# Optimization experiments

Hardware: AMD Instinct MI355X
Metric: run time of the kernel (lower is better)

Reference implementation:

```python
import jax, jax.numpy as jnp
import numpy as np

D_MODEL = 128
D_STATE = 16
BATCH = 4
SEQ = 4096
LOG_CLAMP = 70.0  # numeric floor used by the original (use_double=False path)


def setup_inputs() -> dict:
    key = jax.random.key(0)
    ks = jax.random.split(key, 10)
    sd = 1.0 / np.sqrt(D_MODEL)
    x = jax.random.normal(ks[0], (BATCH, SEQ, D_MODEL), dtype=jnp.float32)
    # Araw: kaiming-normal then clamped at min=-4
    Araw = jnp.clip(jax.random.normal(ks[1], (D_MODEL, D_STATE), dtype=jnp.float32) * np.sqrt(2.0 / D_MODEL), -4.0, None)
    P = jax.random.normal(ks[2], (D_MODEL,), dtype=jnp.float32)
    W_B = jax.random.normal(ks[3], (D_MODEL, D_STATE), dtype=jnp.float32) * sd
    b_B = jax.random.normal(ks[4], (D_STATE,), dtype=jnp.float32) * sd
    W_C = jax.random.normal(ks[5], (D_MODEL, D_STATE), dtype=jnp.float32) * sd
    b_C = jax.random.normal(ks[6], (D_STATE,), dtype=jnp.float32) * sd
    W_D = jax.random.normal(ks[7], (D_MODEL, 1), dtype=jnp.float32) * sd
    b_D = jax.random.normal(ks[8], (1,), dtype=jnp.float32) * sd
    return {"x": x, "Araw": Araw, "P": P, "W_B": W_B, "b_B": b_B,
            "W_C": W_C, "b_C": b_C, "W_D": W_D, "b_D": b_D}


def reference(x, Araw, P, W_B, b_B, W_C, b_C, W_D, b_D):
    sp = jax.nn.softplus
    # disc: [B,S,D] -- s_D(x) is [B,S,1], repeated across d_model == broadcast
    disc = sp(P + (x @ W_D + b_D))
    A = -sp(Araw)                          # [D,N], strictly negative
    A_bar_pre = disc[..., None] * A        # [B,S,D,N] (log of A_bar)
    A_bar = jnp.exp(A_bar_pre)             # [B,S,D,N]
    Bm = x @ W_B + b_B                     # [B,S,N]
    B_bar = Bm[:, :, None, :] / A * (A_bar - 1.0)  # [B,S,D,N]
    C = x @ W_C + b_C                      # [B,S,N]

    # log-space parallel scan (pref_sum path, use_double=False)
    Bx = B_bar * x[..., None]              # [B,S,D,N]
    Bx_log = jnp.log(jnp.abs(Bx))
    A_bar_prod_log = jnp.cumsum(A_bar_pre, axis=1)          # inclusive prefix sum of logs
    A_bar_prod_log = jnp.maximum(A_bar_prod_log, Bx_log - LOG_CLAMP)
    AinvsB = jnp.exp(Bx_log - A_bar_prod_log) * jnp.sign(Bx)
    AinvsBsum = jnp.cumsum(AinvsB, axis=1)
    h = AinvsBsum * jnp.exp(A_bar_prod_log)                 # [B,S,D,N]
    y = jnp.einsum('bsdn,bsn->bsd', h, C)                   # [B,S,D]
    return y
```

## Files before the change

### kernel.cpp

```cpp
#include <hip/hip_runtime.h>
#include <math.h>

#define B_ 4
#define S_ 4096
#define D_ 128
#define N_ 16
#define CHUNK_ 64
#define NCHUNK_ (S_ / CHUNK_)
#define NCHAN_ (B_ * D_ * N_)
#define KC_ 8
#define KNC_ (S_ / KC_)

#define CAPF  3.0e38f
#define LOG2E 1.4426950408889634f
#define C70F  100.98865286222744f

__device__ __forceinline__ float fast_sp(float z) {
    return fmaxf(z, 0.0f) + __logf(1.0f + __expf(-fabsf(z)));
}

__device__ __forceinline__ float exp2_hw(float x) {
#if __has_builtin(__builtin_amdgcn_exp2f)
    return __builtin_amdgcn_exp2f(x);
#else
    return exp2f(x);
#endif
}

template<int CTRL>
__device__ __forceinline__ float dpp_radd(float v) {
    int o = __builtin_amdgcn_mov_dpp(__float_as_int(v), CTRL, 0xf, 0xf, true);
    return v + __int_as_float(o);
}

__device__ __forceinline__ float dpp_reduce16(float v) {
    v = dpp_radd<0x121>(v);
    v = dpp_radd<0x122>(v);
    v = dpp_radd<0x124>(v);
    v = dpp_radd<0x128>(v);
    return v;
}

__global__ __launch_bounds__(256) void k1_proj(
    const float* __restrict__ x,
    const float* __restrict__ W_B, const float* __restrict__ b_B,
    const float* __restrict__ W_C, const float* __restrict__ b_C,
    const float* __restrict__ W_D, const float* __restrict__ b_D,
    float* __restrict__ xWD, float* __restrict__ BmT, float* __restrict__ CmT)
{
    __shared__ float xs[16][132];
    __shared__ float sB[16][17], sC[16][17];
    const int row0 = blockIdx.x * 16;
    const int b  = row0 >> 12;
    const int t0 = row0 & (S_ - 1);
    const int tid = threadIdx.x;

    {
        const float4* xsrc = (const float4*)(x + (size_t)row0 * D_);
        int i0 = tid * 2;
        float4 v0 = xsrc[i0];
        float4 v1 = xsrc[i0 + 1];
        int r = i0 >> 5;
        int c = (i0 << 2) & 127;
        *(float4*)&xs[r][c]     = v0;
        *(float4*)&xs[r][c + 4] = v1;
    }
    __syncthreads();

    const int r = tid >> 4;
    const int n = tid & 15;
    float a = 0.f, c = 0.f;
    #pragma unroll 4
    for (int k = 0; k < D_; ++k) {
        float xv = xs[r][k];
        a = fmaf(xv, W_B[k * N_ + n], a);
        c = fmaf(xv, W_C[k * N_ + n], c);
    }
    sB[n][r] = a + b_B[n];
    sC[n][r] = c + b_C[n];

    if (tid < 16) {
        float dsum = 0.f;
        #pragma unroll 4
        for (int k = 0; k < D_; ++k) dsum = fmaf(xs[tid][k], W_D[k], dsum);
        xWD[row0 + tid] = dsum + b_D[0];
    }
    __syncthreads();

    const int n2 = tid >> 4, r2 = tid & 15;
    BmT[(size_t)(b * N_ + n2) * S_ + t0 + r2] = sB[n2][r2];
    CmT[(size_t)(b * N_ + n2) * S_ + t0 + r2] = sC[n2][r2];
}

__global__ __launch_bounds__(512) void kS(
    const float* __restrict__ xWD, const float* __restrict__ P,
    float* __restrict__ dstart)
{
    __shared__ float wtot[8];
    const int bd = blockIdx.x;
    const int b = bd >> 7, d = bd & (D_ - 1);
    const float Pd = P[d];
    const int c = threadIdx.x;
    const int lane = c & 63, wv = c >> 6;

    const float4* xw = (const float4*)(xWD + b * S_) + c * 2;
    float4 a0 = xw[0], a1 = xw[1];
    float s = fast_sp(Pd + a0.x) + fast_sp(Pd + a0.y)
            + fast_sp(Pd + a0.z) + fast_sp(Pd + a0.w)
            + fast_sp(Pd + a1.x) + fast_sp(Pd + a1.y)
            + fast_sp(Pd + a1.z) + fast_sp(Pd + a1.w);
    float sc = s;
    #pragma unroll
    for (int off = 1; off < 64; off <<= 1) {
        float o = __shfl_up(sc, off);
        if (lane >= off) sc += o;
    }
    if (lane == 63) wtot[wv] = sc;
    __syncthreads();
    float base = 0.f;
    #pragma unroll
    for (int i = 0; i < 7; ++i)
        if (i < wv) base += wtot[i];
    dstart[bd * KNC_ + c] = base + sc - s;
}

template <int PHASE_C>
__global__ __launch_bounds__(256, 8) void k3_scan(
    const float* __restrict__ x, const float* __restrict__ Araw,
    const float* __restrict__ P, const float* __restrict__ xWD,
    const float* __restrict__ BmT, const float* __restrict__ CmT,
    const float* __restrict__ dstart,
    float* __restrict__ csum,
    float* __restrict__ y)
{
    __shared__ __align__(16) float lds[PHASE_C ? 5 * 1024 : 3 * 1024 + 64];
    float* ld_x = lds;
    float* ld_b = lds + 1024;
    float* ld_d = lds + 2048;
    float* ld_c = lds + (PHASE_C ? 3072 : 0);
    float* ld_y = lds + (PHASE_C ? 4096 : 0);

    const int blk = blockIdx.x;
    const int dg = blk & 7;
    const int ch = (blk >> 3) & (NCHUNK_ - 1);
    const int b  = blk >> 9;
    const int tid = threadIdx.x;
    const int lane = tid & 63;
    const int w = tid >> 6;
    const int n  = tid & 15;
    const int dl = tid >> 4;
    const int d  = dg * 16 + dl;
    const int bd = b * D_ + d;
    const int cid = bd * N_ + n;
    const int t0 = ch * CHUNK_;

    float carry = 0.f;
    if (PHASE_C) {
        float p0 = 0.f, p1 = 0.f, p2 = 0.f, p3 = 0.f;
        int k = 0;
        for (; k + 4 <= ch; k += 4) {
            p0 += csum[(size_t)(k + 0) * NCHAN_ + cid];
            p1 += csum[(size_t)(k + 1) * NCHAN_ + cid];
            p2 += csum[(size_t)(k + 2) * NCHAN_ + cid];
            p3 += csum[(size_t)(k + 3) * NCHAN_ + cid];
        }
        for (; k < ch; ++k) p0 += csum[(size_t)k * NCHAN_ + cid];
        carry = (p0 + p1) + (p2 + p3);
    }

    if (w == 0) {
        const float* src = x + ((size_t)b * S_ + t0) * D_ + dg * 16;
        #pragma unroll
        for (int it = 0; it < 4; ++it) {
            int g = it * 64 + lane;
            int t = g >> 2, dq = g & 3;
            float4 v = *(const float4*)(src + (size_t)t * D_ + dq * 4);
            int t4 = t >> 2, tl = t & 3;
            const float va[4] = {v.x, v.y, v.z, v.w};
            #pragma unroll
            for (int j = 0; j < 4; ++j) {
                int dd = dq * 4 + j;
                ld_x[dd * 64 + ((t4 ^ (dd & 7)) << 2) + tl] = va[j];
            }
        }
    } else if (w == 1) {
        const float* src = BmT + (size_t)(b * N_) * S_ + t0;
        #pragma unroll
        for (int it = 0; it < 4; ++it) {
            int g = it * 64 + lane;
            int row = g >> 4, t16 = g & 15;
            int tlog = t16 ^ (row & 7);
            *(float4*)&ld_b[row * 64 + t16 * 4] =
                *(const float4*)(src + (size_t)row * S_ + tlog * 4);
        }
    } else if (PHASE_C && w == 2) {
        const float* src = CmT + (size_t)(b * N_) * S_ + t0;
        #pragma unroll
        for (int it = 0; it < 4; ++it) {
            int g = it * 64 + lane;
            int row = g >> 4, t16 = g & 15;
            int tlog = t16 ^ (row & 7);
            *(float4*)&ld_c[row * 64 + t16 * 4] =
                *(const float4*)(src + (size_t)row * S_ + tlog * 4);
        }
    } else if (w == (PHASE_C ? 3 : 2)) {
        float v = xWD[b * S_ + t0 + lane];
        int t4 = lane >> 2, tl = lane & 3;
        #pragma unroll
        for (int dl2 = 0; dl2 < 16; ++dl2) {
            float sp = fast_sp(P[dg * 16 + dl2] + v);
            ld_d[dl2 * 64 + ((t4 ^ (dl2 & 7)) << 2) + tl] = sp;
        }
    }
    __syncthreads();

    if (!PHASE_C) {
        unsigned long long* mk = (unsigned long long*)(lds + 3072);
        #pragma unroll
        for (int i = 0; i < 4; ++i) {
            int rr = w * 4 + i;
            int idx = rr * 64 + ((((lane >> 2) ^ (rr & 7)) << 2) | (lane & 3));
            unsigned long long mx = __ballot((__float_as_uint(ld_x[idx]) >> 31) & 1);
            unsigned long long mb = __ballot((__float_as_uint(ld_b[idx]) >> 31) & 1);
            if (lane == 0) { mk[rr] = mx; mk[16 + rr] = mb; }
        }
        __syncthreads();
    }

    const float A  = -fast_sp(Araw[d * N_ + n]);
    const float rA = 1.0f / A;
    const float A2 = A * LOG2E;

    const float cum0 = fmaf(A2, dstart[bd * KNC_ + ch * (CHUNK_ / KC_)], C70F);
    float cum2 = cum0;
    float run = carry;

    const int sdl = dl & 7, sn = n & 7;
    const int offd_base = dl * 64;
    const int offn_base = n * 64;

    const bool fastp = __all(cum0 <= -128.0f);

    if (fastp) {
        if (!PHASE_C) {
            const unsigned long long* mk =
                (const unsigned long long*)(lds + 3072);
            int pc = (int)__popcll(mk[dl] ^ mk[16 + n]);
            run += (float)(64 - 2 * pc);
        } else {
            #pragma unroll 2
            for (int t4 = 0; t4 < CHUNK_ / 4; ++t4) {
                const int od = offd_base + ((t4 ^ sdl) << 2);
                const int on = offn_base + ((t4 ^ sn) << 2);
                float4 dv = *(const float4*)&ld_d[od];
                float4 xv = *(const float4*)&ld_x[od];
                float4 bv = *(const float4*)&ld_b[on];
                float4 Cv = *(const float4*)&ld_c[on];
                const float dva[4] = {dv.x, dv.y, dv.z, dv.w};
                const float xva[4] = {xv.x, xv.y, xv.z, xv.w};
                const float bva[4] = {bv.x, bv.y, bv.z, bv.w};
                const float Cva[4] = {Cv.x, Cv.y, Cv.z, Cv.w};
                #pragma unroll
                for (int j = 0; j < 4; ++j) {
                    float ab  = exp2_hw(dva[j] * A2);
                    float ww  = fmaf(ab, xva[j], -xva[j]);
                    float Bx  = (bva[j] * rA) * ww;
                    run += copysignf(1.0f, Bx);
                    float yv = run * fabsf(Bx) * Cva[j];
                    yv = dpp_reduce16(yv);
                    if (n == 0) ld_y[(t4 * 4 + j) * 16 + dl] = yv;
                }
            }
        }
    } else {
        #pragma unroll 2
        for (int t4 = 0; t4 < CHUNK_ / 4; ++t4) {
            const int od = offd_base + ((t4 ^ sdl) << 2);
            const int on = offn_base + ((t4 ^ sn) << 2);
            float4 dv = *(const float4*)&ld_d[od];
            float4 xv = *(const float4*)&ld_x[od];
            float4 bv = *(const float4*)&ld_b[on];
            float4 Cv;
            if (PHASE_C) Cv = *(const float4*)&ld_c[on];

            const float dva[4] = {dv.x, dv.y, dv.z, dv.w};
            const float xva[4] = {xv.x, xv.y, xv.z, xv.w};
            const float bva[4] = {bv.x, bv.y, bv.z, bv.w};
            const float Cva[4] = {Cv.x, Cv.y, Cv.z, Cv.w};

            #pragma unroll
            for (int j = 0; j < 4; ++j) {
                float t1 = dva[j] * A2;
                cum2 += t1;
                float ab  = exp2_hw(t1);
                float ww  = fmaf(ab, xva[j], -xva[j]);
                float Bx  = (bva[j] * rA) * ww;
                float aBx = fabsf(Bx);
                float en  = fminf(exp2_hw(-cum2), CAPF);
                float m   = aBx * en;
                float mag = fminf(m, 1.0f);
                run += copysignf(mag, Bx);
                if (PHASE_C) {
                    float ecl = aBx * __builtin_amdgcn_rcpf(fmaxf(mag, 1e-37f));
                    float yv = run * ecl * Cva[j];
                    yv = dpp_reduce16(yv);
                    if (n == 0) ld_y[(t4 * 4 + j) * 16 + dl] = yv;
                }
            }
        }
    }

    if (!PHASE_C) {
        csum[(size_t)ch * NCHAN_ + cid] = run;
    } else {
        __syncthreads();
        int t  = tid >> 2;
        int dp = tid & 3;
        float4 v = *(const float4*)&ld_y[t * 16 + dp * 4];
        *(float4*)&y[((size_t)b * S_ + t0 + t) * D_ + dg * 16 + dp * 4] = v;
    }
}

extern "C" void kernel_launch(void* const* d_in, const int* in_sizes, int n_in,
                              void* d_out, int out_size, void* d_ws, size_t ws_size,
                              hipStream_t stream)
{
    const float* x    = (const float*)d_in[0];
    const float* Araw = (const float*)d_in[1];
    const float* P    = (const float*)d_in[2];
    const float* W_B  = (const float*)d_in[3];
    const float* b_B  = (const float*)d_in[4];
    const float* W_C  = (const float*)d_in[5];
    const float* b_C  = (const float*)d_in[6];
    const float* W_D  = (const float*)d_in[7];
    const float* b_D  = (const float*)d_in[8];
    float* y  = (float*)d_out;
    float* ws = (float*)d_ws;

    float* xWD    = ws;
    float* BmT    = xWD  + B_ * S_;
    float* CmT    = BmT  + B_ * S_ * N_;
    float* dstart = CmT  + B_ * S_ * N_;
    float* csum   = dstart + B_ * D_ * KNC_;

    hipLaunchKernelGGL(k1_proj, dim3(B_ * S_ / 16), dim3(256), 0, stream,
                       x, W_B, b_B, W_C, b_C, W_D, b_D, xWD, BmT, CmT);
    hipLaunchKernelGGL(kS, dim3(B_ * D_), dim3(512), 0, stream,
                       xWD, P, dstart);
    hipLaunchKernelGGL((k3_scan<0>), dim3(B_ * NCHUNK_ * (D_ / 16)), dim3(256), 0, stream,
                       x, Araw, P, xWD, BmT, CmT, dstart, csum, y);
    hipLaunchKernelGGL((k3_scan<1>), dim3(B_ * NCHUNK_ * (D_ / 16)), dim3(256), 0, stream,
                       x, Araw, P, xWD, BmT, CmT, dstart, csum, y);
}
```

Before: 60.39 us.

## Fuse two scan phases into one cooperative kernel with grid sync

Merges the chunk-sum phase and the output phase of the scan into a single cooperative kernel separated by a grid-wide barrier. Inputs stay staged in LDS across both phases instead of being reloaded by a second launch. The aim is to save one kernel launch plus the repeated global-to-LDS staging. In exchange it pays for a grid sync across 2048 blocks and host-side occupancy queries on every call, and it falls back to the old two-kernel path if a cooperative launch is not possible.

After: 60.57 us. Within noise of the previous version (+0.3%).

```diff
diff --git a/kernel.cpp b/kernel.cpp
--- a/kernel.cpp
+++ b/kernel.cpp
@@ -1,5 +1,8 @@
 #include <hip/hip_runtime.h>
+#include <hip/hip_cooperative_groups.h>
 #include <math.h>
+
+namespace cg = cooperative_groups;
 
 #define B_ 4
 #define S_ 4096
@@ -7,6 +10,7 @@
 #define N_ 16
 #define CHUNK_ 64
 #define NCHUNK_ (S_ / CHUNK_)
+#define NTASK_ (B_ * 8 * NCHUNK_)
 #define NCHAN_ (B_ * D_ * N_)
 #define KC_ 8
 #define KNC_ (S_ / KC_)
@@ -124,8 +128,53 @@
     dstart[bd * KNC_ + c] = base + sc - s;
 }
 
-template <int PHASE_C>
-__global__ __launch_bounds__(256, 8) void k3_scan(
+__device__ __forceinline__ void stage_x(
+    const float* __restrict__ x, float* ld_x,
+    int b, int t0, int dg, int lane)
+{
+    const float* src = x + ((size_t)b * S_ + t0) * D_ + dg * 16;
+    #pragma unroll
+    for (int it = 0; it < 4; ++it) {
+        int g = it * 64 + lane;
+        int t = g >> 2, dq = g & 3;
+        float4 v = *(const float4*)(src + (size_t)t * D_ + dq * 4);
+        int t4 = t >> 2, tl = t & 3;
+        const float va[4] = {v.x, v.y, v.z, v.w};
+        #pragma unroll
+        for (int j = 0; j < 4; ++j) {
+            int dd = dq * 4 + j;
+            ld_x[dd * 64 + ((t4 ^ (dd & 7)) << 2) + tl] = va[j];
+        }
+    }
+}
+
+__device__ __forceinline__ void stage_rowmajor(
+    const float* __restrict__ src, float* dst, int lane)
+{
+    #pragma unroll
+    for (int it = 0; it < 4; ++it) {
+        int g = it * 64 + lane;
+        int row = g >> 4, t16 = g & 15;
+        int tlog = t16 ^ (row & 7);
+        *(float4*)&dst[row * 64 + t16 * 4] =
+            *(const float4*)(src + (size_t)row * S_ + tlog * 4);
+    }
+}
+
+__device__ __forceinline__ void stage_disc(
+    const float* __restrict__ xWD, const float* __restrict__ P,
+    float* ld_d, int b, int t0, int dg, int lane)
+{
+    float v = xWD[b * S_ + t0 + lane];
+    int t4 = lane >> 2, tl = lane & 3;
+    #pragma unroll
+    for (int dl2 = 0; dl2 < 16; ++dl2) {
+        float sp = fast_sp(P[dg * 16 + dl2] + v);
+        ld_d[dl2 * 64 + ((t4 ^ (dl2 & 7)) << 2) + tl] = sp;
+    }
+}
+
+__global__ __launch_bounds__(256, 8) void k3_fused(
     const float* __restrict__ x, const float* __restrict__ Araw,
     const float* __restrict__ P, const float* __restrict__ xWD,
     const float* __restrict__ BmT, const float* __restrict__ CmT,
@@ -133,12 +182,12 @@
     float* __restrict__ csum,
     float* __restrict__ y)
 {
-    __shared__ __align__(16) float lds[PHASE_C ? 5 * 1024 : 3 * 1024 + 64];
+    __shared__ __align__(16) float lds[5 * 1024];
     float* ld_x = lds;
     float* ld_b = lds + 1024;
     float* ld_d = lds + 2048;
-    float* ld_c = lds + (PHASE_C ? 3072 : 0);
-    float* ld_y = lds + (PHASE_C ? 4096 : 0);
+    float* ld_c = lds + 3072;
+    float* ld_y = lds + 4096;
 
     const int blk = blockIdx.x;
     const int dg = blk & 7;
@@ -154,6 +203,185 @@
     const int cid = bd * N_ + n;
     const int t0 = ch * CHUNK_;
 
+    if (w == 0)      stage_x(x, ld_x, b, t0, dg, lane);
+    else if (w == 1) stage_rowmajor(BmT + (size_t)(b * N_) * S_ + t0, ld_b, lane);
+    else if (w == 2) stage_rowmajor(CmT + (size_t)(b * N_) * S_ + t0, ld_c, lane);
+    else             stage_disc(xWD, P, ld_d, b, t0, dg, lane);
+    __syncthreads();
+
+    {
+        unsigned long long* mk = (unsigned long long*)ld_y;
+        #pragma unroll
+        for (int i = 0; i < 4; ++i) {
+            int rr = w * 4 + i;
+            int idx = rr * 64 + ((((lane >> 2) ^ (rr & 7)) << 2) | (lane & 3));
+            unsigned long long mx = __ballot((__float_as_uint(ld_x[idx]) >> 31) & 1);
+            unsigned long long mb = __ballot((__float_as_uint(ld_b[idx]) >> 31) & 1);
+            if (lane == 0) { mk[rr] = mx; mk[16 + rr] = mb; }
+        }
+        __syncthreads();
+    }
+
+    const float A  = -fast_sp(Araw[d * N_ + n]);
+    const float rA = 1.0f / A;
+    const float A2 = A * LOG2E;
+    const float cum0 = fmaf(A2, dstart[bd * KNC_ + ch * (CHUNK_ / KC_)], C70F);
+
+    const int sdl = dl & 7, sn = n & 7;
+    const int offd_base = dl * 64;
+    const int offn_base = n * 64;
+    const bool fastp = __all(cum0 <= -128.0f);
+
+    {
+        float run0 = 0.f;
+        if (fastp) {
+            const unsigned long long* mk = (const unsigned long long*)ld_y;
+            int pc = (int)__popcll(mk[dl] ^ mk[16 + n]);
+            run0 = (float)(64 - 2 * pc);
+        } else {
+            float cum2 = cum0;
+            #pragma unroll 2
+            for (int t4 = 0; t4 < CHUNK_ / 4; ++t4) {
+                const int od = offd_base + ((t4 ^ sdl) << 2);
+                const int on = offn_base + ((t4 ^ sn) << 2);
+                float4 dv = *(const float4*)&ld_d[od];
+                float4 xv = *(const float4*)&ld_x[od];
+                float4 bv = *(const float4*)&ld_b[on];
+                const float dva[4] = {dv.x, dv.y, dv.z, dv.w};
+                const float xva[4] = {xv.x, xv.y, xv.z, xv.w};
+                const float bva[4] = {bv.x, bv.y, bv.z, bv.w};
+                #pragma unroll
+                for (int j = 0; j < 4; ++j) {
+                    float t1 = dva[j] * A2;
+                    cum2 += t1;
+                    float ab  = exp2_hw(t1);
+                    float ww  = fmaf(ab, xva[j], -xva[j]);
+                    float Bx  = (bva[j] * rA) * ww;
+                    float en  = fminf(exp2_hw(-cum2), CAPF);
+                    float m   = fabsf(Bx) * en;
+                    run0 += copysignf(fminf(m, 1.0f), Bx);
+                }
+            }
+        }
+        csum[(size_t)ch * NCHAN_ + cid] = run0;
+    }
+
+    __threadfence();
+    cg::this_grid().sync();
+    __threadfence();
+
+    float carry = 0.f;
+    {
+        float p0 = 0.f, p1 = 0.f, p2 = 0.f, p3 = 0.f;
+        int k = 0;
+        for (; k + 4 <= ch; k += 4) {
+            p0 += csum[(size_t)(k + 0) * NCHAN_ + cid];
+            p1 += csum[(size_t)(k + 1) * NCHAN_ + cid];
+            p2 += csum[(size_t)(k + 2) * NCHAN_ + cid];
+            p3 += csum[(size_t)(k + 3) * NCHAN_ + cid];
+        }
+        for (; k < ch; ++k) p0 += csum[(size_t)k * NCHAN_ + cid];
+        carry = (p0 + p1) + (p2 + p3);
+    }
+
+    float run = carry;
+    float cum2 = cum0;
+    if (fastp) {
+        #pragma unroll 2
+        for (int t4 = 0; t4 < CHUNK_ / 4; ++t4) {
+            const int od = offd_base + ((t4 ^ sdl) << 2);
+            const int on = offn_base + ((t4 ^ sn) << 2);
+            float4 dv = *(const float4*)&ld_d[od];
+            float4 xv = *(const float4*)&ld_x[od];
+            float4 bv = *(const float4*)&ld_b[on];
+            float4 Cv = *(const float4*)&ld_c[on];
+            const float dva[4] = {dv.x, dv.y, dv.z, dv.w};
+            const float xva[4] = {xv.x, xv.y, xv.z, xv.w};
+            const float bva[4] = {bv.x, bv.y, bv.z, bv.w};
+            const float Cva[4] = {Cv.x, Cv.y, Cv.z, Cv.w};
+            #pragma unroll
+            for (int j = 0; j < 4; ++j) {
+                float ab  = exp2_hw(dva[j] * A2);
+                float ww  = fmaf(ab, xva[j], -xva[j]);
+                float Bx  = (bva[j] * rA) * ww;
+                run += copysignf(1.0f, Bx);
+                float yv = run * fabsf(Bx) * Cva[j];
+                yv = dpp_reduce16(yv);
+                if (n == 0) ld_y[(t4 * 4 + j) * 16 + dl] = yv;
+            }
+        }
+    } else {
+        #pragma unroll 2
+        for (int t4 = 0; t4 < CHUNK_ / 4; ++t4) {
+            const int od = offd_base + ((t4 ^ sdl) << 2);
+            const int on = offn_base + ((t4 ^ sn) << 2);
+            float4 dv = *(const float4*)&ld_d[od];
+            float4 xv = *(const float4*)&ld_x[od];
+            float4 bv = *(const float4*)&ld_b[on];
+            float4 Cv = *(const float4*)&ld_c[on];
+            const float dva[4] = {dv.x, dv.y, dv.z, dv.w};
+            const float xva[4] = {xv.x, xv.y, xv.z, xv.w};
+            const float bva[4] = {bv.x, bv.y, bv.z, bv.w};
+            const float Cva[4] = {Cv.x, Cv.y, Cv.z, Cv.w};
+            #pragma unroll
+            for (int j = 0; j < 4; ++j) {
+                float t1 = dva[j] * A2;
+                cum2 += t1;
+                float ab  = exp2_hw(t1);
+                float ww  = fmaf(ab, xva[j], -xva[j]);
+                float Bx  = (bva[j] * rA) * ww;
+                float aBx = fabsf(Bx);
+                float en  = fminf(exp2_hw(-cum2), CAPF);
+                float m   = aBx * en;
+                float mag = fminf(m, 1.0f);
+                run += copysignf(mag, Bx);
+                float ecl = aBx * __builtin_amdgcn_rcpf(fmaxf(mag, 1e-37f));
+                float yv = run * ecl * Cva[j];
+                yv = dpp_reduce16(yv);
+                if (n == 0) ld_y[(t4 * 4 + j) * 16 + dl] = yv;
+            }
+        }
+    }
+
+    __syncthreads();
+    {
+        int t  = tid >> 2;
+        int dp = tid & 3;
+        float4 v = *(const float4*)&ld_y[t * 16 + dp * 4];
+        *(float4*)&y[((size_t)b * S_ + t0 + t) * D_ + dg * 16 + dp * 4] = v;
+    }
+}
+
+template <int PHASE_C>
+__global__ __launch_bounds__(256, 8) void k3_scan(
+    const float* __restrict__ x, const float* __restrict__ Araw,
+    const float* __restrict__ P, const float* __restrict__ xWD,
+    const float* __restrict__ BmT, const float* __restrict__ CmT,
+    const float* __restrict__ dstart,
+    float* __restrict__ csum,
+    float* __restrict__ y)
+{
+    __shared__ __align__(16) float lds[PHASE_C ? 5 * 1024 : 3 * 1024 + 64];
+    float* ld_x = lds;
+    float* ld_b = lds + 1024;
+    float* ld_d = lds + 2048;
+    float* ld_c = lds + (PHASE_C ? 3072 : 0);
+    float* ld_y = lds + (PHASE_C ? 4096 : 0);
+
+    const int blk = blockIdx.x;
+    const int dg = blk & 7;
+    const int ch = (blk >> 3) & (NCHUNK_ - 1);
+    const int b  = blk >> 9;
+    const int tid = threadIdx.x;
+    const int lane = tid & 63;
+    const int w = tid >> 6;
+    const int n  = tid & 15;
+    const int dl = tid >> 4;
+    const int d  = dg * 16 + dl;
+    const int bd = b * D_ + d;
+    const int cid = bd * N_ + n;
+    const int t0 = ch * CHUNK_;
+
     float carry = 0.f;
     if (PHASE_C) {
         float p0 = 0.f, p1 = 0.f, p2 = 0.f, p3 = 0.f;
@@ -168,50 +396,12 @@
         carry = (p0 + p1) + (p2 + p3);
     }
 
-    if (w == 0) {
-        const float* src = x + ((size_t)b * S_ + t0) * D_ + dg * 16;
-        #pragma unroll
-        for (int it = 0; it < 4; ++it) {
-            int g = it * 64 + lane;
-            int t = g >> 2, dq = g & 3;
-            float4 v = *(const float4*)(src + (size_t)t * D_ + dq * 4);
-            int t4 = t >> 2, tl = t & 3;
-            const float va[4] = {v.x, v.y, v.z, v.w};
-            #pragma unroll
-            for (int j = 0; j < 4; ++j) {
-                int dd = dq * 4 + j;
-                ld_x[dd * 64 + ((t4 ^ (dd & 7)) << 2) + tl] = va[j];
-            }
-        }
-    } else if (w == 1) {
-        const float* src = BmT + (size_t)(b * N_) * S_ + t0;
-        #pragma unroll
-        for (int it = 0; it < 4; ++it) {
-            int g = it * 64 + lane;
-            int row = g >> 4, t16 = g & 15;
-            int tlog = t16 ^ (row & 7);
-            *(float4*)&ld_b[row * 64 + t16 * 4] =
-                *(const float4*)(src + (size_t)row * S_ + tlog * 4);
-        }
-    } else if (PHASE_C && w == 2) {
-        const float* src = CmT + (size_t)(b * N_) * S_ + t0;
-        #pragma unroll
-        for (int it = 0; it < 4; ++it) {
-            int g = it * 64 + lane;
-            int row = g >> 4, t16 = g & 15;
-            int tlog = t16 ^ (row & 7);
-            *(float4*)&ld_c[row * 64 + t16 * 4] =
-                *(const float4*)(src + (size_t)row * S_ + tlog * 4);
-        }
-    } else if (w == (PHASE_C ? 3 : 2)) {
-        float v = xWD[b * S_ + t0 + lane];
-        int t4 = lane >> 2, tl = lane & 3;
-        #pragma unroll
-        for (int dl2 = 0; dl2 < 16; ++dl2) {
-            float sp = fast_sp(P[dg * 16 + dl2] + v);
-            ld_d[dl2 * 64 + ((t4 ^ (dl2 & 7)) << 2) + tl] = sp;
-        }
-    }
+    if (w == 0)      stage_x(x, ld_x, b, t0, dg, lane);
+    else if (w == 1) stage_rowmajor(BmT + (size_t)(b * N_) * S_ + t0, ld_b, lane);
+    else if (PHASE_C && w == 2)
+                     stage_rowmajor(CmT + (size_t)(b * N_) * S_ + t0, ld_c, lane);
+    else if (w == (PHASE_C ? 3 : 2))
+                     stage_disc(xWD, P, ld_d, b, t0, dg, lane);
     __syncthreads();
 
     if (!PHASE_C) {
@@ -230,7 +420,6 @@
     const float A  = -fast_sp(Araw[d * N_ + n]);
     const float rA = 1.0f / A;
     const float A2 = A * LOG2E;
-
     const float cum0 = fmaf(A2, dstart[bd * KNC_ + ch * (CHUNK_ / KC_)], C70F);
     float cum2 = cum0;
     float run = carry;
@@ -238,7 +427,6 @@
     const int sdl = dl & 7, sn = n & 7;
     const int offd_base = dl * 64;
     const int offn_base = n * 64;
-
     const bool fastp = __all(cum0 <= -128.0f);
 
     if (fastp) {
@@ -282,12 +470,10 @@
             float4 bv = *(const float4*)&ld_b[on];
             float4 Cv;
             if (PHASE_C) Cv = *(const float4*)&ld_c[on];
-
             const float dva[4] = {dv.x, dv.y, dv.z, dv.w};
             const float xva[4] = {xv.x, xv.y, xv.z, xv.w};
             const float bva[4] = {bv.x, bv.y, bv.z, bv.w};
             const float Cva[4] = {Cv.x, Cv.y, Cv.z, Cv.w};
-
             #pragma unroll
             for (int j = 0; j < 4; ++j) {
                 float t1 = dva[j] * A2;
@@ -347,8 +533,28 @@
                        x, W_B, b_B, W_C, b_C, W_D, b_D, xWD, BmT, CmT);
     hipLaunchKernelGGL(kS, dim3(B_ * D_), dim3(512), 0, stream,
                        xWD, P, dstart);
-    hipLaunchKernelGGL((k3_scan<0>), dim3(B_ * NCHUNK_ * (D_ / 16)), dim3(256), 0, stream,
-                       x, Araw, P, xWD, BmT, CmT, dstart, csum, y);
-    hipLaunchKernelGGL((k3_scan<1>), dim3(B_ * NCHUNK_ * (D_ / 16)), dim3(256), 0, stream,
-                       x, Araw, P, xWD, BmT, CmT, dstart, csum, y);
-}
+
+    int dev = 0;
+    hipGetDevice(&dev);
+    int coop = 0, numCU = 0, maxB = 0;
+    hipDeviceGetAttribute(&coop, hipDeviceAttributeCooperativeLaunch, dev);
+    hipDeviceGetAttribute(&numCU, hipDeviceAttributeMultiprocessorCount, dev);
+    hipOccupancyMaxActiveBlocksPerMultiprocessor(&maxB, k3_fused, 256, 0);
+
+    bool useCoop = coop && ((long)maxB * numCU >= NTASK_);
+    if (useCoop) {
+        void* args[] = {(void*)&x, (void*)&Araw, (void*)&P, (void*)&xWD,
+                        (void*)&BmT, (void*)&CmT, (void*)&dstart,
+                        (void*)&csum, (void*)&y};
+        hipError_t e = hipLaunchCooperativeKernel(
+            reinterpret_cast<void*>(k3_fused), dim3(NTASK_), dim3(256),
+            args, 0, stream);
+        if (e != hipSuccess) useCoop = false;
+    }
+    if (!useCoop) {
+        hipLaunchKernelGGL((k3_scan<0>), dim3(NTASK_), dim3(256), 0, stream,
+                           x, Araw, P, xWD, BmT, CmT, dstart, csum, y);
+        hipLaunchKernelGGL((k3_scan<1>), dim3(NTASK_), dim3(256), 0, stream,
+                           x, Araw, P, xWD, BmT, CmT, dstart, csum, y);
+    }
+}
```
